# Kernel optimization log

Measured on AMD Instinct MI355X. Metric: run time of the kernel, lower is better.

## Reference

```python
import jax, jax.numpy as jnp
import numpy as np

N_WIRES = 8
DIM = 2 ** N_WIRES  # 256


def _rx(theta):
    # theta: [] or [N] -> [2,2] or [N,2,2] complex64
    c = jnp.cos(theta / 2)
    s = jnp.sin(theta / 2)
    return jnp.stack([jnp.stack([c + 0j, -1j * s], -1),
                      jnp.stack([-1j * s, c + 0j], -1)], -2)


def _ry(theta):
    c = jnp.cos(theta / 2)
    s = jnp.sin(theta / 2)
    return jnp.stack([jnp.stack([c + 0j, -s + 0j], -1),
                      jnp.stack([s + 0j, c + 0j], -1)], -2)


def _rz(theta):
    e = jnp.exp(-1j * theta / 2)
    z = jnp.zeros_like(e)
    return jnp.stack([jnp.stack([e, z], -1),
                      jnp.stack([z, jnp.conj(e)], -1)], -2)


def _apply_1q(state, U, wire):
    # state: [N, DIM]; U: [2,2] (shared) or [N,2,2] (per-sample)
    s = state.reshape(-1, 2 ** wire, 2, 2 ** (N_WIRES - 1 - wire))
    if U.ndim == 2:
        s = jnp.einsum('ab,nxby->nxay', U, s)
    else:
        s = jnp.einsum('nab,nxby->nxay', U, s)
    return s.reshape(-1, DIM)


def _cnot(state, c, t):
    # wire 0 = most significant bit (PennyLane convention)
    s = state.reshape((-1,) + (2,) * N_WIRES)
    ax_c = 1 + c
    s0 = jnp.take(s, 0, axis=ax_c)
    s1 = jnp.take(s, 1, axis=ax_c)
    ax_t = 1 + t if t < c else t  # target axis after control axis removed
    s1 = jnp.flip(s1, axis=ax_t)
    s = jnp.stack([s0, s1], axis=ax_c)
    return s.reshape(-1, DIM)


def _z_signs():
    idx = np.arange(DIM)
    bits = (idx[:, None] >> (N_WIRES - 1 - np.arange(N_WIRES))[None, :]) & 1
    return jnp.asarray(1.0 - 2.0 * bits, dtype=jnp.float32)  # [DIM, 8]


def _circuit(x_flat, params):
    # x_flat: [N, 8] angles; params: [8, 3]
    n = x_flat.shape[0]
    state = jnp.zeros((n, DIM), dtype=jnp.complex64).at[:, 0].set(1.0)
    for i in range(N_WIRES):
        state = _apply_1q(state, _rx(x_flat[:, i]), i)
    for i in range(N_WIRES):
        state = _apply_1q(state, _ry(params[i, 0]), i)
        state = _apply_1q(state, _rz(params[i, 1]), i)
        state = _apply_1q(state, _rx(params[i, 2]), i)
    for i in range(N_WIRES - 1):
        state = _cnot(state, i, i + 1)
    state = _cnot(state, N_WIRES - 1, 0)
    probs = state.real ** 2 + state.imag ** 2  # [N, DIM]
    return probs @ _z_signs()  # [N, 8] PauliZ expvals


def setup_inputs() -> dict:
    key = jax.random.key(0)
    ks = jax.random.split(key, 4)
    B, S = 16, 2048
    embed_dim, ffn_dim = 512, 2048
    return {
        'x': jax.random.normal(ks[0], (B, S, N_WIRES), dtype=jnp.float32),
        'params': jax.random.normal(ks[1], (N_WIRES, 3), dtype=jnp.float32),
        'W1': jax.random.normal(ks[2], (ffn_dim, N_WIRES), dtype=jnp.float32) * 0.1,
        'b1': jnp.zeros((ffn_dim,), dtype=jnp.float32),
        'W2': jax.random.normal(ks[3], (embed_dim, ffn_dim), dtype=jnp.float32) * 0.02,
        'b2': jnp.zeros((embed_dim,), dtype=jnp.float32),
    }


def reference(x, params, W1, b1, W2, b2):
    B, S, _ = x.shape
    ev = _circuit(x.reshape(-1, N_WIRES), params).reshape(B, S, N_WIRES)
    h = jax.nn.relu(ev @ W1.T + b1)
    return h @ W2.T + b2
```

## Files before the change

### kernel.cpp

```cpp
#include <hip/hip_runtime.h>
#include <hip/hip_bf16.h>

#define NS 32768
#define EMB 512
#define KDIM 2048
#define BM 256
#define BN 128
#define NITER (KDIM / 32)

typedef float f32x16 __attribute__((ext_vector_type(16)));
typedef __bf16 bf16x8 __attribute__((ext_vector_type(8)));
typedef __bf16 bf16x2 __attribute__((ext_vector_type(2)));
typedef unsigned int u32;
typedef const __attribute__((address_space(1))) u32* gptr_t;
typedef __attribute__((address_space(3))) u32* lptr_t;

__device__ __forceinline__ void gload_lds16(const void* g, void* l) {
    __builtin_amdgcn_global_load_lds((gptr_t)g, (lptr_t)l, 16, 0, 0);
}

__device__ __forceinline__ u32 pkrelu(float lo, float hi) {
    union { bf16x2 h; u32 u; } c;
    c.h[0] = (__bf16)fmaxf(lo, 0.f);
    c.h[1] = (__bf16)fmaxf(hi, 0.f);
    return c.u;
}

__device__ __forceinline__ bf16x8 mk_af(u32 a, u32 b, u32 c, u32 d) {
    union { u32 u[4]; bf16x8 v; } t;
    t.u[0] = a; t.u[1] = b; t.u[2] = c; t.u[3] = d;
    return t.v;
}

__device__ __forceinline__ void h_to_af(const f32x16 h, bf16x8& af0, bf16x8& af1) {
    af0 = mk_af(pkrelu(h[0], h[1]),  pkrelu(h[2], h[3]),
                pkrelu(h[4], h[5]),  pkrelu(h[6], h[7]));
    af1 = mk_af(pkrelu(h[8], h[9]),  pkrelu(h[10], h[11]),
                pkrelu(h[12], h[13]), pkrelu(h[14], h[15]));
}

__global__ __launch_bounds__(256) void k_prep(const float* __restrict__ W2,
                                              const float* __restrict__ W1,
                                              __hip_bfloat16* __restrict__ W2b,
                                              __hip_bfloat16* __restrict__ W1bg) {
    int t = threadIdx.x;
    if (blockIdx.x < 1024) {
        int i = (blockIdx.x * 256 + t) * 4;
        float4 v = *(const float4*)(W2 + i);
        __hip_bfloat16 o[4];
        o[0] = __float2bfloat16(v.x); o[1] = __float2bfloat16(v.y);
        o[2] = __float2bfloat16(v.z); o[3] = __float2bfloat16(v.w);
        *(ulong1*)(W2b + i) = *(ulong1*)o;
    } else {
        int j = (blockIdx.x - 1024) * 1024 + t * 4;
        float4 w = *(const float4*)(W1 + j);
        __hip_bfloat16 p[4];
        p[0] = __float2bfloat16(w.x); p[1] = __float2bfloat16(w.y);
        p[2] = __float2bfloat16(w.z); p[3] = __float2bfloat16(w.w);
        *(ulong1*)(W1bg + j) = *(ulong1*)p;
    }
}

__global__ __launch_bounds__(512, 4) void k_gemm(
        const float* __restrict__ x,
        const float* __restrict__ params,
        const __hip_bfloat16* __restrict__ W1bg,
        const float* __restrict__ b1,
        const __hip_bfloat16* __restrict__ W2b,
        const float* __restrict__ b2,
        float* __restrict__ C) {
    __shared__ __hip_bfloat16 Bs[2][8 * 512];
    __shared__ __hip_bfloat16 W1s[KDIM * 8];
    __shared__ __hip_bfloat16 b1h[KDIM];
    __shared__ __hip_bfloat16 evs[BM * 8];

    int tid = threadIdx.x, wave = tid >> 6, lane = tid & 63;
    int l31 = lane & 31, half = lane >> 5;
    int bx = blockIdx.x, bm = bx >> 2, bn = bx & 3;

    if (tid < 256) {
        float K1[8], K2[8];
        #pragma unroll
        for (int i = 0; i < 8; i++) {
            float a = params[i*3+0], b = params[i*3+1], g = params[i*3+2];
            float sa, ca, sb, cb, sg, cg;
            __sincosf(a, &sa, &ca);
            __sincosf(b, &sb, &cb);
            __sincosf(g, &sg, &cg);
            K1[i] = sa*sb*sg + ca*cg;
            K2[i] = cb*sg;
        }
        int n = bm * BM + tid;
        float4 x0 = *(const float4*)(x + (size_t)n*8);
        float4 x1 = *(const float4*)(x + (size_t)n*8 + 4);
        float xs[8] = {x0.x, x0.y, x0.z, x0.w, x1.x, x1.y, x1.z, x1.w};
        float z[8];
        #pragma unroll
        for (int i = 0; i < 8; i++) {
            float s, c;
            __sincosf(xs[i], &s, &c);
            z[i] = c * K1[i] - s * K2[i];
        }
        float evv[8];
        float p = z[0];
        #pragma unroll
        for (int j = 1; j < 8; j++) { p *= z[j]; evv[j] = p; }
        float sfx = z[7];
        #pragma unroll
        for (int j = 6; j >= 1; j--) sfx *= z[j];
        evv[0] = sfx;
        __hip_bfloat16 o[8];
        #pragma unroll
        for (int i = 0; i < 8; i++) o[i] = __float2bfloat16(evv[i]);
        *(bf16x8*)&evs[tid * 8] = *(bf16x8*)o;
    }
    for (int i = tid; i < KDIM; i += 512) {
        int q = (i >> 2) & 3;
        int src = i + ((q == 1) ? 4 : (q == 2) ? -4 : 0);
        *(bf16x8*)&W1s[i * 8] = *(const bf16x8*)(W1bg + (size_t)src * 8);
        b1h[i] = __float2bfloat16(b1[src]);
    }

    const __hip_bfloat16* gBp =
        W2b + (size_t)(bn*BN + (wave >> 1)*32 + l31) * KDIM + (wave & 1)*16 + half*8;
    gload_lds16(gBp, &Bs[0][wave * 512]);
    gBp += 32;

    __syncthreads();

    bf16x8 evB;
    if (half == 0) {
        evB = *(bf16x8*)&evs[(wave * 32 + l31) * 8];
    } else {
        evB = (bf16x8){};
        evB[0] = (__bf16)1.0f;
    }
    const f32x16 z16 = {};

    f32x16 acc[4] = {};

#define COMPUTE_AF(K0, A0, A1) do {                                           \
        bf16x8 w1f;                                                           \
        if (half == 0) {                                                      \
            w1f = *(const bf16x8*)&W1s[((K0) + l31) * 8];                     \
        } else {                                                              \
            w1f = (bf16x8){};                                                 \
            w1f[0] = *(const __bf16*)&b1h[(K0) + l31];                        \
        }                                                                     \
        f32x16 h = __builtin_amdgcn_mfma_f32_32x32x16_bf16(w1f, evB, z16, 0, 0, 0); \
        h_to_af(h, A0, A1);                                                   \
    } while (0)

#define GEMM2_STEP(CB, A0, A1) do {                                           \
        __builtin_amdgcn_s_setprio(1);                                        \
        _Pragma("unroll")                                                     \
        for (int ni = 0; ni < 4; ni++) {                                      \
            bf16x8 bf0 = *(bf16x8*)&Bs[CB][(ni*2 + 0) * 512 + lane * 8];      \
            acc[ni] = __builtin_amdgcn_mfma_f32_32x32x16_bf16(A0, bf0, acc[ni], 0, 0, 0); \
            bf16x8 bf1 = *(bf16x8*)&Bs[CB][(ni*2 + 1) * 512 + lane * 8];      \
            acc[ni] = __builtin_amdgcn_mfma_f32_32x32x16_bf16(A1, bf1, acc[ni], 0, 0, 0); \
        }                                                                     \
        __builtin_amdgcn_s_setprio(0);                                        \
    } while (0)

    bf16x8 aA0, aA1;
    bf16x8 aB0, aB1;
    COMPUTE_AF(0, aA0, aA1);

    for (int it = 0; it < NITER; it += 2) {
        gload_lds16(gBp, &Bs[1][wave * 512]);
        gBp += 32;
        COMPUTE_AF((it + 1) * 32, aB0, aB1);
        GEMM2_STEP(0, aA0, aA1);
        __syncthreads();

        if (it + 2 < NITER) {
            gload_lds16(gBp, &Bs[0][wave * 512]);
            gBp += 32;
            COMPUTE_AF((it + 2) * 32, aA0, aA1);
        }
        GEMM2_STEP(1, aB0, aB1);
        __syncthreads();
    }
#undef COMPUTE_AF
#undef GEMM2_STEP

    int rbase = bm*BM + wave*32 + 4*half;
    #pragma unroll
    for (int ni = 0; ni < 4; ni++) {
        int col = bn*BN + ni*32 + l31;
        float bias = b2[col];
        #pragma unroll
        for (int r = 0; r < 16; r++) {
            int row = rbase + (r & 3) + 8 * (r >> 2);
            C[(size_t)row * EMB + col] = acc[ni][r] + bias;
        }
    }
}

extern "C" void kernel_launch(void* const* d_in, const int* in_sizes, int n_in,
                              void* d_out, int out_size, void* d_ws, size_t ws_size,
                              hipStream_t stream) {
    const float* x      = (const float*)d_in[0];
    const float* params = (const float*)d_in[1];
    const float* W1     = (const float*)d_in[2];
    const float* b1     = (const float*)d_in[3];
    const float* W2     = (const float*)d_in[4];
    const float* b2     = (const float*)d_in[5];
    float* out = (float*)d_out;

    char* ws = (char*)d_ws;
    __hip_bfloat16* W2b  = (__hip_bfloat16*)ws;
    __hip_bfloat16* W1bg = (__hip_bfloat16*)(ws + 2097152);

    k_prep<<<1040, 256, 0, stream>>>(W2, W1, W2b, W1bg);
    k_gemm<<<(NS/BM) * (EMB/BN), 512, 0, stream>>>(x, params, W1bg, b1, W2b, b2, out);
}
```

Before: 150.6 us.

## Load W2 fragments directly from global into registers, halve block rows

Drops the LDS double-buffered staging of W2 via global_load_lds and its per-step barriers. Each wave now loads its B fragments straight from global memory into registers inside an unrolled loop. Block size shrinks to 128 rows with 256 threads and launch bounds become (256,3). This removes LDS traffic and synchronisation, but every wave now fetches the full B tile independently, so global/L2 traffic per block rises and there is no explicit prefetch overlap.

```diff
diff --git a/kernel.cpp b/kernel.cpp
--- a/kernel.cpp
+++ b/kernel.cpp
@@ -4,7 +4,7 @@
 #define NS 32768
 #define EMB 512
 #define KDIM 2048
-#define BM 256
+#define BM 128
 #define BN 128
 #define NITER (KDIM / 32)
 
@@ -12,12 +12,6 @@
 typedef __bf16 bf16x8 __attribute__((ext_vector_type(8)));
 typedef __bf16 bf16x2 __attribute__((ext_vector_type(2)));
 typedef unsigned int u32;
-typedef const __attribute__((address_space(1))) u32* gptr_t;
-typedef __attribute__((address_space(3))) u32* lptr_t;
-
-__device__ __forceinline__ void gload_lds16(const void* g, void* l) {
-    __builtin_amdgcn_global_load_lds((gptr_t)g, (lptr_t)l, 16, 0, 0);
-}
 
 __device__ __forceinline__ u32 pkrelu(float lo, float hi) {
     union { bf16x2 h; u32 u; } c;
@@ -61,7 +55,7 @@
     }
 }
 
-__global__ __launch_bounds__(512, 4) void k_gemm(
+__global__ __launch_bounds__(256, 3) void k_gemm(
         const float* __restrict__ x,
         const float* __restrict__ params,
         const __hip_bfloat16* __restrict__ W1bg,
@@ -69,7 +63,6 @@
         const __hip_bfloat16* __restrict__ W2b,
         const float* __restrict__ b2,
         float* __restrict__ C) {
-    __shared__ __hip_bfloat16 Bs[2][8 * 512];
     __shared__ __hip_bfloat16 W1s[KDIM * 8];
     __shared__ __hip_bfloat16 b1h[KDIM];
     __shared__ __hip_bfloat16 evs[BM * 8];
@@ -78,7 +71,7 @@
     int l31 = lane & 31, half = lane >> 5;
     int bx = blockIdx.x, bm = bx >> 2, bn = bx & 3;
 
-    if (tid < 256) {
+    if (tid < 128) {
         float K1[8], K2[8];
         #pragma unroll
         for (int i = 0; i < 8; i++) {
@@ -114,17 +107,19 @@
         for (int i = 0; i < 8; i++) o[i] = __float2bfloat16(evv[i]);
         *(bf16x8*)&evs[tid * 8] = *(bf16x8*)o;
     }
-    for (int i = tid; i < KDIM; i += 512) {
+    for (int i = tid; i < KDIM; i += 256) {
         int q = (i >> 2) & 3;
         int src = i + ((q == 1) ? 4 : (q == 2) ? -4 : 0);
         *(bf16x8*)&W1s[i * 8] = *(const bf16x8*)(W1bg + (size_t)src * 8);
         b1h[i] = __float2bfloat16(b1[src]);
     }
 
-    const __hip_bfloat16* gBp =
-        W2b + (size_t)(bn*BN + (wave >> 1)*32 + l31) * KDIM + (wave & 1)*16 + half*8;
-    gload_lds16(gBp, &Bs[0][wave * 512]);
-    gBp += 32;
+    const __hip_bfloat16* pf[8];
+    #pragma unroll
+    for (int f = 0; f < 8; f++) {
+        int ni = f >> 1, t = f & 1;
+        pf[f] = W2b + (size_t)(bn*BN + ni*32 + l31) * KDIM + t*16 + half*8;
+    }
 
     __syncthreads();
 
@@ -139,51 +134,38 @@
 
     f32x16 acc[4] = {};
 
-#define COMPUTE_AF(K0, A0, A1) do {                                           \
-        bf16x8 w1f;                                                           \
-        if (half == 0) {                                                      \
-            w1f = *(const bf16x8*)&W1s[((K0) + l31) * 8];                     \
-        } else {                                                              \
-            w1f = (bf16x8){};                                                 \
-            w1f[0] = *(const __bf16*)&b1h[(K0) + l31];                        \
-        }                                                                     \
-        f32x16 h = __builtin_amdgcn_mfma_f32_32x32x16_bf16(w1f, evB, z16, 0, 0, 0); \
-        h_to_af(h, A0, A1);                                                   \
-    } while (0)
-
-#define GEMM2_STEP(CB, A0, A1) do {                                           \
-        __builtin_amdgcn_s_setprio(1);                                        \
-        _Pragma("unroll")                                                     \
-        for (int ni = 0; ni < 4; ni++) {                                      \
-            bf16x8 bf0 = *(bf16x8*)&Bs[CB][(ni*2 + 0) * 512 + lane * 8];      \
-            acc[ni] = __builtin_amdgcn_mfma_f32_32x32x16_bf16(A0, bf0, acc[ni], 0, 0, 0); \
-            bf16x8 bf1 = *(bf16x8*)&Bs[CB][(ni*2 + 1) * 512 + lane * 8];      \
-            acc[ni] = __builtin_amdgcn_mfma_f32_32x32x16_bf16(A1, bf1, acc[ni], 0, 0, 0); \
-        }                                                                     \
-        __builtin_amdgcn_s_setprio(0);                                        \
-    } while (0)
-
-    bf16x8 aA0, aA1;
-    bf16x8 aB0, aB1;
-    COMPUTE_AF(0, aA0, aA1);
-
-    for (int it = 0; it < NITER; it += 2) {
-        gload_lds16(gBp, &Bs[1][wave * 512]);
-        gBp += 32;
-        COMPUTE_AF((it + 1) * 32, aB0, aB1);
-        GEMM2_STEP(0, aA0, aA1);
-        __syncthreads();
-
-        if (it + 2 < NITER) {
-            gload_lds16(gBp, &Bs[0][wave * 512]);
-            gBp += 32;
-            COMPUTE_AF((it + 2) * 32, aA0, aA1);
-        }
-        GEMM2_STEP(1, aB0, aB1);
-        __syncthreads();
-    }
-#undef COMPUTE_AF
-#undef GEMM2_STEP
+    for (int it0 = 0; it0 < NITER; it0 += 8) {
+        #pragma unroll
+        for (int un = 0; un < 8; un++) {
+            const int k0 = (it0 + un) * 32;
+
+            bf16x8 bf[8];
+            #pragma unroll
+            for (int f = 0; f < 8; f++)
+                bf[f] = *(const bf16x8*)(pf[f] + un * 32);
+
+            bf16x8 w1f;
+            if (half == 0) {
+                w1f = *(const bf16x8*)&W1s[(k0 + l31) * 8];
+            } else {
+                w1f = (bf16x8){};
+                w1f[0] = *(const __bf16*)&b1h[k0 + l31];
+            }
+            f32x16 h = __builtin_amdgcn_mfma_f32_32x32x16_bf16(w1f, evB, z16, 0, 0, 0);
+            bf16x8 af0, af1;
+            h_to_af(h, af0, af1);
+
+            __builtin_amdgcn_s_setprio(1);
+            #pragma unroll
+            for (int ni = 0; ni < 4; ni++) {
+                acc[ni] = __builtin_amdgcn_mfma_f32_32x32x16_bf16(af0, bf[ni*2 + 0], acc[ni], 0, 0, 0);
+                acc[ni] = __builtin_amdgcn_mfma_f32_32x32x16_bf16(af1, bf[ni*2 + 1], acc[ni], 0, 0, 0);
+            }
+            __builtin_amdgcn_s_setprio(0);
+        }
+        #pragma unroll
+        for (int f = 0; f < 8; f++) pf[f] += 8 * 32;
+    }
 
     int rbase = bm*BM + wave*32 + 4*half;
     #pragma unroll
@@ -214,5 +196,5 @@
     __hip_bfloat16* W1bg = (__hip_bfloat16*)(ws + 2097152);
 
     k_prep<<<1040, 256, 0, stream>>>(W2, W1, W2b, W1bg);
-    k_gemm<<<(NS/BM) * (EMB/BN), 512, 0, stream>>>(x, params, W1bg, b1, W2b, b2, out);
-}
+    k_gemm<<<(NS/BM) * (EMB/BN), 256, 0, stream>>>(x, params, W1bg, b1, W2b, b2, out);
+}
```

After: 312.7 us. 108% more time.
